# Kernel optimization log

Measured on AMD Instinct MI355X. Metric: run time of the kernel, lower is better.

## Reference

```python
import jax, jax.numpy as jnp
import numpy as np

B, T, N, F = 8, 32, 10000, 16
E = 160000
HG, HT = 64, 128
EPS = 1e-5


def setup_inputs() -> dict:
    key = jax.random.key(0)
    ks = jax.random.split(key, 12)
    s = lambda i, shape, sc=0.05: jax.random.normal(ks[i], shape, dtype=jnp.float32) * sc
    return {
        "x_seq": jax.random.normal(ks[0], (B, T, N, F), dtype=jnp.float32),
        "edge_index": jax.random.randint(ks[1], (2, E), 0, N),
        "W1l": s(2, (HG, F)), "b1": jnp.zeros((HG,), jnp.float32), "W1r": s(3, (HG, F)),
        "g1": jnp.ones((HG,), jnp.float32), "be1": jnp.zeros((HG,), jnp.float32),
        "W2l": s(4, (HG, HG)), "b2": jnp.zeros((HG,), jnp.float32), "W2r": s(5, (HG, HG)),
        "g2": jnp.ones((HG,), jnp.float32), "be2": jnp.zeros((HG,), jnp.float32),
        "W_ih": s(6, (3 * HT, HG)), "W_hh": s(7, (3 * HT, HT)),
        "b_ih": jnp.zeros((3 * HT,), jnp.float32), "b_hh": jnp.zeros((3 * HT,), jnp.float32),
        "Wh": s(8, (1, HT)), "bh": jnp.zeros((1,), jnp.float32),
    }


def _layernorm(h, g, b):
    mu = h.mean(-1, keepdims=True)
    var = ((h - mu) ** 2).mean(-1, keepdims=True)
    return (h - mu) * jax.lax.rsqrt(var + EPS) * g + b


def reference(x_seq, edge_index, W1l, b1, W1r, g1, be1, W2l, b2, W2r, g2, be2,
              W_ih, W_hh, b_ih, b_hh, Wh, bh):
    src, dst = edge_index[0], edge_index[1]
    deg = jax.ops.segment_sum(jnp.ones((E,), x_seq.dtype), dst, num_segments=N)
    inv_deg = (1.0 / jnp.maximum(deg, 1.0))[:, None]  # [N,1]

    def aggregate(x):  # x: [B,N,F] -> mean over incoming neighbors per node
        msgs = x[:, src, :]  # [B,E,F] gather
        agg = jax.vmap(lambda m: jax.ops.segment_sum(m, dst, num_segments=N))(msgs)
        return agg * inv_deg

    def sage(x, Wl, bl, Wr, g, b):
        # PyG SAGEConv(mean): lin_l(agg) + lin_r(x); then LayerNorm + ReLU (dropout=eval)
        h = aggregate(x) @ Wl.T + bl + x @ Wr.T
        return jax.nn.relu(_layernorm(h, g, b))

    def step(_, xt):  # xt: [B,N,F] -> pooled [B,HG]
        h = sage(xt, W1l, b1, W1r, g1, be1)
        h = sage(h, W2l, b2, W2r, g2, be2)
        return None, h.mean(axis=1)

    _, H = jax.lax.scan(step, None, jnp.swapaxes(x_seq, 0, 1))  # [T,B,HG]

    def gru_step(h, x):  # PyTorch GRU gate order: r, z, n
        gi = x @ W_ih.T + b_ih
        gh = h @ W_hh.T + b_hh
        ir, iz, in_ = jnp.split(gi, 3, axis=-1)
        hr, hz, hn = jnp.split(gh, 3, axis=-1)
        r = jax.nn.sigmoid(ir + hr)
        z = jax.nn.sigmoid(iz + hz)
        n = jnp.tanh(in_ + r * hn)
        return (1.0 - z) * n + z * h, None

    h0 = jnp.zeros((x_seq.shape[0], HT), x_seq.dtype)
    ht, _ = jax.lax.scan(gru_step, h0, H)
    return (ht @ Wh.T + bh).squeeze(-1)  # [B]
```

## Files before the change

### kernel.cpp

```cpp
#include <hip/hip_runtime.h>
#include <hip/hip_fp16.h>
#include <math.h>

#define B_ 8
#define T_ 32
#define N_ 10000
#define F_ 16
#define E_ 160000
#define HG_ 64
#define HT_ 128
#define BT_ (B_*T_)
#define PB_ 157
#define EPS_ 1e-5f
#define NR_ (N_+1)

typedef __attribute__((ext_vector_type(8))) _Float16 f16x8_t;
typedef __attribute__((ext_vector_type(4))) float f32x4_t;

__device__ inline unsigned short f2h(float f) {
  return __half_as_ushort(__float2half(f));
}
__device__ inline unsigned pkrtz_u(float a, float b) {
  auto h = __builtin_amdgcn_cvt_pkrtz(a, b);
  unsigned u; __builtin_memcpy(&u, &h, 4); return u;
}
__device__ inline unsigned pack2h(float a, float b) {
  __half2 h = __floats2half2_rn(a, b);
  unsigned u; __builtin_memcpy(&u, &h, 4); return u;
}
__device__ inline __half2 u2h(unsigned u) {
  __half2 h; __builtin_memcpy(&h, &u, 4); return h;
}
__device__ inline unsigned h2u(__half2 h) {
  unsigned u; __builtin_memcpy(&u, &h, 4); return u;
}
__device__ inline void bflyh(__half2& a, int m) {
  unsigned u = (unsigned)__shfl_xor((int)h2u(a), m);
  a += u2h(u);
}

__global__ void k_zero(int* p, int n) {
  int i = blockIdx.x * 256 + threadIdx.x;
  if (i < n) p[i] = 0;
}

__global__ void k_deg(const int* __restrict__ dst, int* __restrict__ deg) {
  int e = blockIdx.x * 256 + threadIdx.x;
  if (e < E_) atomicAdd(&deg[dst[e]], 1);
}

__global__ void k_scan(const int* __restrict__ deg, int* __restrict__ row_ptr,
                       float* __restrict__ inv_deg) {
  __shared__ int part[256];
  int tid = threadIdx.x;
  int base = tid * 40;
  int s = 0;
  for (int i = 0; i < 40; i++) { int idx = base + i; if (idx < N_) s += deg[idx]; }
  part[tid] = s;
  __syncthreads();
  if (tid == 0) {
    int run = 0;
    for (int i = 0; i < 256; i++) { int v = part[i]; part[i] = run; run += v; }
  }
  __syncthreads();
  int run = part[tid];
  for (int i = 0; i < 40; i++) {
    int idx = base + i;
    if (idx < N_) {
      row_ptr[idx] = run;
      int d = deg[idx];
      run += d;
      inv_deg[idx] = 1.0f / fmaxf((float)d, 1.0f);
    } else if (idx == N_) {
      row_ptr[N_] = run;
    }
  }
}

__global__ void k_fill(const int* __restrict__ src, const int* __restrict__ dst,
                       const int* __restrict__ row_ptr, int* __restrict__ cursor,
                       int* __restrict__ col) {
  int e = blockIdx.x * 256 + threadIdx.x;
  if (e < E_) {
    int d = dst[e];
    int p = atomicAdd(&cursor[d], 1);
    col[row_ptr[d] + p] = src[e];
  }
}

__global__ void k_prepw(const float* __restrict__ W2l, const float* __restrict__ W2r,
                        unsigned short* __restrict__ Wbf) {
  int idx = blockIdx.x * 256 + threadIdx.x;
  if (idx >= 4 * 4 * 64 * 8) return;
  int q  = idx & 7;
  int l  = (idx >> 3) & 63;
  int ks = (idx >> 9) & 3;
  int w  = idx >> 11;
  int j = w * 16 + (l & 15);
  int k = ks * 32 + ((l >> 4) * 8) + q;
  float v = (k < 64) ? W2l[j * 64 + k] : W2r[j * 64 + (k - 64)];
  Wbf[idx] = f2h(v);
}

__global__ void k_prepw1(const float* __restrict__ W1l, const float* __restrict__ W1r,
                         unsigned short* __restrict__ Wb1) {
  int idx = blockIdx.x * 256 + threadIdx.x;
  if (idx >= 4 * 64 * 8) return;
  int q = idx & 7;
  int l = (idx >> 3) & 63;
  int w = idx >> 9;
  int j = w * 16 + (l & 15);
  int k = ((l >> 4) * 8) + q;
  float v = (k < 16) ? W1l[j * 16 + k] : W1r[j * 16 + (k - 16)];
  Wb1[idx] = f2h(v);
}

__launch_bounds__(256, 8)
__global__ void k_sage1t(const float* __restrict__ x, const int* __restrict__ row_ptr,
                         const int* __restrict__ col, const float* __restrict__ inv_deg,
                         const unsigned short* __restrict__ Wb1, const float* __restrict__ b1,
                         const float* __restrict__ g1, const float* __restrict__ be1,
                         unsigned short* __restrict__ h1, const float* __restrict__ zrow,
                         int bt0, int CH, int swz) {
  __shared__ __align__(16) unsigned short ZU[64 * 136];
  __shared__ float red[2][4][64];
  unsigned short* Z1b = ZU;
  float* Zf = (float*)ZU;
  int i = blockIdx.x;
  int btl, chunk;
  if (swz) {
    int xcd = i & 7; int j = i >> 3; int per = CH >> 3;
    btl = xcd * per + j / PB_; chunk = j % PB_;
  } else {
    btl = i / PB_; chunk = i % PB_;
  }
  int bt = bt0 + btl;
  size_t xbase = (size_t)bt * (N_ * F_);
  int tid = threadIdx.x;
  int w = __builtin_amdgcn_readfirstlane(tid >> 6);
  int lane = tid & 63;
  int n0 = chunk * 64;
  int node = lane >> 4;
  int eo2 = (lane >> 2) & 3;
  int fq2 = lane & 3;
  const float4* x4b = (const float4*)(x + xbase);
  const float4* z4 = (const float4*)zrow;

  int nloc = n0 + w * 16 + (lane & 15);
  int rpA = 0, dS = 0; float ivS = 0.f;
  if (nloc < N_) { rpA = row_ptr[nloc]; dS = row_ptr[nloc + 1] - rpA; ivS = inv_deg[nloc]; }

  for (int p = 0; p < 4; ++p) {
    int mA = w * 16 + p * 4;
    int nA = n0 + mA;
    int s0My   = __shfl(rpA, p * 4 + node);
    int dMy    = __shfl(dS,  p * 4 + node);
    float ivMy = __shfl(ivS, p * 4 + node);
    int dcMy = dMy > 64 ? 64 : dMy;
    int tmx = max(dcMy, __shfl_xor(dcMy, 16));
    int mx  = max(tmx, __shfl_xor(tmx, 32));
    int rounds = (mx + 3) >> 2;
    int pos = lane & 15;
    int c0r = (pos      < dMy) ? col[s0My + pos]      : 0;
    int c1r = (pos + 16 < dMy) ? col[s0My + pos + 16] : 0;
    int c2r = (pos + 32 < dMy) ? col[s0My + pos + 32] : 0;
    int c3r = (pos + 48 < dMy) ? col[s0My + pos + 48] : 0;
    float4 a = {0.f, 0.f, 0.f, 0.f};
#define S1B(REG, BASE, RR)                                            \
    {                                                                 \
      int idx = eo2 + 4 * (RR);                                       \
      int s = __shfl(REG, (lane & 48) | (idx - (BASE)));              \
      const float4* bp = (idx < dcMy) ? (x4b + (size_t)s * 4) : z4;   \
      float4 v = bp[fq2];                                             \
      a.x += v.x; a.y += v.y; a.z += v.z; a.w += v.w;                 \
    }
    int rounds2 = (rounds + 1) & ~1;
    int r = 0;
    for (; r < rounds2 && r < 4;  r += 2) { S1B(c0r, 0, r)  S1B(c0r, 0, r + 1) }
    for (; r < rounds2 && r < 8;  r += 2) { S1B(c1r, 16, r) S1B(c1r, 16, r + 1) }
    for (; r < rounds2 && r < 12; r += 2) { S1B(c2r, 32, r) S1B(c2r, 32, r + 1) }
    for (; r < rounds2; r += 2)           { S1B(c3r, 48, r) S1B(c3r, 48, r + 1) }
#undef S1B
    if (dMy > 64) {
      for (int e = s0My + 64; e < s0My + dMy; ++e) {
        if (eo2 == 0) {
          float4 v = x4b[(size_t)col[e] * 4 + fq2];
          a.x += v.x; a.y += v.y; a.z += v.z; a.w += v.w;
        }
      }
    }
    a.x += __shfl_xor(a.x, 4);  a.y += __shfl_xor(a.y, 4);
    a.z += __shfl_xor(a.z, 4);  a.w += __shfl_xor(a.w, 4);
    a.x += __shfl_xor(a.x, 8);  a.y += __shfl_xor(a.y, 8);
    a.z += __shfl_xor(a.z, 8);  a.w += __shfl_xor(a.w, 8);
    if (eo2 == 0) {
      uint2 pk;
      pk.x = pkrtz_u(a.x * ivMy, a.y * ivMy);
      pk.y = pkrtz_u(a.z * ivMy, a.w * ivMy);
      *(uint2*)&Z1b[(mA + node) * 40 + fq2 * 4] = pk;
    } else if (eo2 == 1) {
      int nS = nA + node;
      float4 sv = {0.f, 0.f, 0.f, 0.f};
      if (nS < N_) sv = x4b[(size_t)nS * 4 + fq2];
      uint2 pk;
      pk.x = pkrtz_u(sv.x, sv.y);
      pk.y = pkrtz_u(sv.z, sv.w);
      *(uint2*)&Z1b[(mA + node) * 40 + 16 + fq2 * 4] = pk;
    }
  }
  __syncthreads();

  int g = lane >> 4, c = lane & 15;
  float bj = b1[w * 16 + c];
  f32x4_t accf[4];
#pragma unroll
  for (int mt = 0; mt < 4; ++mt) accf[mt] = (f32x4_t){bj, bj, bj, bj};
  f16x8_t bfr = ((const f16x8_t*)Wb1)[w * 64 + lane];
#pragma unroll
  for (int mt = 0; mt < 4; ++mt) {
    const f16x8_t* ap = (const f16x8_t*)&Z1b[(mt * 16 + c) * 40 + g * 8];
    accf[mt] = __builtin_amdgcn_mfma_f32_16x16x32_f16(*ap, bfr, accf[mt], 0, 0, 0);
  }
  __syncthreads();

#pragma unroll
  for (int mt = 0; mt < 4; ++mt) {
#pragma unroll
    for (int q = 0; q < 4; ++q) {
      int nodeq = mt * 16 + g * 4 + q;
      Zf[nodeq * 68 + w * 16 + c] = accf[mt][q];
    }
  }
  __syncthreads();

  int m = lane;
  const float* zr = Zf + m * 68 + w * 16;
  float4 z0 = *(const float4*)(zr + 0);
  float4 z1 = *(const float4*)(zr + 4);
  float4 z2 = *(const float4*)(zr + 8);
  float4 z3 = *(const float4*)(zr + 12);
  float acc[16];
  acc[0] = z0.x; acc[1] = z0.y; acc[2] = z0.z; acc[3] = z0.w;
  acc[4] = z1.x; acc[5] = z1.y; acc[6] = z1.z; acc[7] = z1.w;
  acc[8] = z2.x; acc[9] = z2.y; acc[10] = z2.z; acc[11] = z2.w;
  acc[12] = z3.x; acc[13] = z3.y; acc[14] = z3.z; acc[15] = z3.w;

  float s1 = 0.f, s2 = 0.f;
#pragma unroll
  for (int jj = 0; jj < 16; ++jj) { s1 += acc[jj]; s2 += acc[jj] * acc[jj]; }
  red[0][w][m] = s1;
  red[1][w][m] = s2;
  __syncthreads();
  float mu = (red[0][0][m] + red[0][1][m] + red[0][2][m] + red[0][3][m]) * (1.f / 64.f);
  float ex2 = (red[1][0][m] + red[1][1][m] + red[1][2][m] + red[1][3][m]) * (1.f / 64.f);
  float var = fmaxf(ex2 - mu * mu, 0.f);
  float rs = rsqrtf(var + EPS_);

  int nAbs = n0 + m;
  unsigned short* dst = h1 + ((size_t)btl * NR_ + nAbs) * HG_ + w * 16;
  if (nAbs < N_) {
#pragma unroll
    for (int jj = 0; jj < 16; ++jj)
      acc[jj] = fmaxf((acc[jj] - mu) * rs * g1[w * 16 + jj] + be1[w * 16 + jj], 0.f);
    uint4 pa, pb;
    pa.x = pack2h(acc[0], acc[1]);  pa.y = pack2h(acc[2], acc[3]);
    pa.z = pack2h(acc[4], acc[5]);  pa.w = pack2h(acc[6], acc[7]);
    pb.x = pack2h(acc[8], acc[9]);  pb.y = pack2h(acc[10], acc[11]);
    pb.z = pack2h(acc[12], acc[13]); pb.w = pack2h(acc[14], acc[15]);
    *(uint4*)dst = pa;
    *(uint4*)(dst + 8) = pb;
  } else if (nAbs == N_) {
    uint4 zz = {0, 0, 0, 0};
    *(uint4*)dst = zz;
    *(uint4*)(dst + 8) = zz;
  }
}

__launch_bounds__(256, 8)
__global__ void k_sage2t(const unsigned short* __restrict__ h1, const int* __restrict__ row_ptr,
                         const int* __restrict__ col, const float* __restrict__ inv_deg,
                         const unsigned short* __restrict__ Wbf, const float* __restrict__ b2,
                         const float* __restrict__ g2, const float* __restrict__ be2,
                         float* __restrict__ Hsum, int bt0, int CH, int swz) {
  __shared__ __align__(16) unsigned short Zb[64 * 136];
  __shared__ float red[2][4][64];
  float* Zf = (float*)Zb;
  int i = blockIdx.x;
  int btl, chunk;
  if (swz) {
    int xcd = i & 7; int j = i >> 3; int per = CH >> 3;
    btl = xcd * per + j / PB_; chunk = j % PB_;
  } else {
    btl = i / PB_; chunk = i % PB_;
  }
  int bt = bt0 + btl;
  int b = bt / T_, t = bt % T_;
  const char* h8c = (const char*)(h1 + (size_t)btl * (NR_ * HG_));
  int tid = threadIdx.x;
  int w = __builtin_amdgcn_readfirstlane(tid >> 6);
  int lane = tid & 63;
  int n0 = chunk * 64;
  int nsel = lane >> 5;
  int eo2 = (lane >> 3) & 3;
  int fq3 = lane & 7;
  unsigned foff = (unsigned)fq3 * 16;
  int pos = lane & 31;

  int nloc = n0 + w * 16 + (lane & 15);
  int rpA = 0, dS = 0; float ivS = 0.f;
  if (nloc < N_) { rpA = row_ptr[nloc]; dS = row_ptr[nloc + 1] - rpA; ivS = inv_deg[nloc]; }

  int cp0[8], cp1[8];
#pragma unroll
  for (int p = 0; p < 8; ++p) {
    int s0 = __shfl(rpA, p * 2 + nsel);
    int d  = __shfl(dS,  p * 2 + nsel);
    cp0[p] = (pos      < d) ? col[s0 + pos]      : N_;
    cp1[p] = (pos + 32 < d) ? col[s0 + pos + 32] : N_;
  }

#pragma unroll
  for (int p = 0; p < 8; ++p) {
    int mA = w * 16 + p * 2;
    int s0My   = __shfl(rpA, p * 2 + nsel);
    int dMy    = __shfl(dS,  p * 2 + nsel);
    float ivMy = __shfl(ivS, p * 2 + nsel);
    int dcMy = dMy > 64 ? 64 : dMy;
    int mx = max(dcMy, __shfl_xor(dcMy, 32));
    int rounds = (mx + 3) >> 2;
    __half2 a0 = __float2half2_rn(0.f), a1 = a0, a2 = a0, a3 = a0;
#define S2B(PREG, BASE, RR)                                             \
    {                                                                   \
      int idx = eo2 + 4 * (RR);                                         \
      int s = __shfl(PREG, (lane & 32) | (idx - (BASE)));               \
      uint4 v = *(const uint4*)(h8c + (((unsigned)s << 7) + foff));     \
      a0 += u2h(v.x); a1 += u2h(v.y); a2 += u2h(v.z); a3 += u2h(v.w);   \
    }
    int rounds2 = (rounds + 1) & ~1;
    int r = 0;
    for (; r < rounds2 && r < 8; r += 2) { S2B(cp0[p], 0, r)  S2B(cp0[p], 0, r + 1) }
    for (; r < rounds2; r += 2)          { S2B(cp1[p], 32, r) S2B(cp1[p], 32, r + 1) }
#undef S2B
    if (dMy > 64) {
      for (int e = s0My + 64; e < s0My + dMy; ++e) {
        if (eo2 == 0) {
          uint4 v = *(const uint4*)(h8c + (((unsigned)col[e] << 7) + foff));
          a0 += u2h(v.x); a1 += u2h(v.y); a2 += u2h(v.z); a3 += u2h(v.w);
        }
      }
    }
    bflyh(a0, 8);  bflyh(a1, 8);  bflyh(a2, 8);  bflyh(a3, 8);
    bflyh(a0, 16); bflyh(a1, 16); bflyh(a2, 16); bflyh(a3, 16);
    if (eo2 == 0) {
      __half2 ivh = __float2half2_rn(ivMy);
      uint4 pk;
      pk.x = h2u(a0 * ivh); pk.y = h2u(a1 * ivh);
      pk.z = h2u(a2 * ivh); pk.w = h2u(a3 * ivh);
      *(uint4*)&Zb[(mA + nsel) * 136 + fq3 * 8] = pk;
    } else if (eo2 == 1) {
      int nA = n0 + mA;
      int nS = nA + nsel;
      int nSc = nS < N_ ? nS : N_;
      uint4 sv = *(const uint4*)(h8c + (((unsigned)nSc << 7) + foff));
      *(uint4*)&Zb[(mA + nsel) * 136 + 64 + fq3 * 8] = sv;
    }
  }
  __syncthreads();

  int g = lane >> 4, c = lane & 15;
  const f16x8_t* Wb8 = (const f16x8_t*)Wbf;
  float bj = b2[w * 16 + c];
  f32x4_t accf[4];
#pragma unroll
  for (int mt = 0; mt < 4; ++mt) accf[mt] = (f32x4_t){bj, bj, bj, bj};
#pragma unroll
  for (int ks = 0; ks < 4; ++ks) {
    f16x8_t bfr = Wb8[(w * 4 + ks) * 64 + lane];
#pragma unroll
    for (int mt = 0; mt < 4; ++mt) {
      const f16x8_t* ap = (const f16x8_t*)&Zb[(mt * 16 + c) * 136 + ks * 32 + g * 8];
      accf[mt] = __builtin_amdgcn_mfma_f32_16x16x32_f16(*ap, bfr, accf[mt], 0, 0, 0);
    }
  }
  __syncthreads();

#pragma unroll
  for (int mt = 0; mt < 4; ++mt) {
#pragma unroll
    for (int q = 0; q < 4; ++q) {
      int nodeq = mt * 16 + g * 4 + q;
      Zf[nodeq * 68 + w * 16 + c] = accf[mt][q];
    }
  }
  __syncthreads();

  int m = lane;
  float* zr = Zf + m * 68 + w * 16;
  float4 z0 = *(const float4*)(zr + 0);
  float4 z1 = *(const float4*)(zr + 4);
  float4 z2 = *(const float4*)(zr + 8);
  float4 z3 = *(const float4*)(zr + 12);
  float acc[16];
  acc[0] = z0.x; acc[1] = z0.y; acc[2] = z0.z; acc[3] = z0.w;
  acc[4] = z1.x; acc[5] = z1.y; acc[6] = z1.z; acc[7] = z1.w;
  acc[8] = z2.x; acc[9] = z2.y; acc[10] = z2.z; acc[11] = z2.w;
  acc[12] = z3.x; acc[13] = z3.y; acc[14] = z3.z; acc[15] = z3.w;

  float s1 = 0.f, s2 = 0.f;
#pragma unroll
  for (int jj = 0; jj < 16; ++jj) { s1 += acc[jj]; s2 += acc[jj] * acc[jj]; }
  red[0][w][m] = s1;
  red[1][w][m] = s2;
  __syncthreads();
  float mu = (red[0][0][m] + red[0][1][m] + red[0][2][m] + red[0][3][m]) * (1.f / 64.f);
  float ex2 = (red[1][0][m] + red[1][1][m] + red[1][2][m] + red[1][3][m]) * (1.f / 64.f);
  float var = fmaxf(ex2 - mu * mu, 0.f);
  float rs = rsqrtf(var + EPS_);

  bool okm = (n0 + m) < N_;
#pragma unroll
  for (int jj = 0; jj < 16; ++jj) {
    float hv = fmaxf((acc[jj] - mu) * rs * g2[w * 16 + jj] + be2[w * 16 + jj], 0.f);
    acc[jj] = okm ? hv : 0.f;
  }
  float4 o0 = {acc[0], acc[1], acc[2], acc[3]};
  float4 o1 = {acc[4], acc[5], acc[6], acc[7]};
  float4 o2 = {acc[8], acc[9], acc[10], acc[11]};
  float4 o3 = {acc[12], acc[13], acc[14], acc[15]};
  *(float4*)(zr + 0) = o0;  *(float4*)(zr + 4) = o1;
  *(float4*)(zr + 8) = o2;  *(float4*)(zr + 12) = o3;
  __syncthreads();

  float cs = 0.f;
#pragma unroll
  for (int ii = 0; ii < 16; ++ii) cs += Zf[(w * 16 + ii) * 68 + lane];
  red[0][w][lane] = cs;
  __syncthreads();
  if (w == 0) {
    float tot = red[0][0][lane] + red[0][1][lane] + red[0][2][lane] + red[0][3][lane];
    atomicAdd(&Hsum[(t * B_ + b) * HG_ + lane], tot);
  }
}

__global__ void k_gi(const float* __restrict__ Hsum, const float* __restrict__ W_ih,
                     const float* __restrict__ b_ih, float* __restrict__ GI) {
  __shared__ float xv[64];
  int tb = blockIdx.x;
  int tid = threadIdx.x;
  if (tid < 64) xv[tid] = Hsum[tb * 64 + tid] * (1.0f / (float)N_);
  __syncthreads();
  float g = b_ih[tid];
  const float4* W4 = (const float4*)(W_ih + tid * 64);
  const float4* x4 = (const float4*)xv;
#pragma unroll
  for (int q = 0; q < 16; q++) {
    float4 w = W4[q], xq = x4[q];
    g = fmaf(xq.x, w.x, g); g = fmaf(xq.y, w.y, g);
    g = fmaf(xq.z, w.z, g); g = fmaf(xq.w, w.w, g);
  }
  GI[tb * 384 + tid] = g;
}

__global__ void k_gru(const float* __restrict__ GI, const float* __restrict__ W_hh,
                      const float* __restrict__ b_hh, const float* __restrict__ Wh,
                      const float* __restrict__ bh, float* __restrict__ out) {
  __shared__ float hL[128];
  __shared__ float ghL[384];
  __shared__ float red[128];
  int b = blockIdx.x, tid = threadIdx.x;
  if (tid < 128) hL[tid] = 0.f;
  float bhh = b_hh[tid];
  const float4* W4 = (const float4*)(W_hh + tid * 128);
  for (int t = 0; t < T_; ++t) {
    __syncthreads();
    float g = bhh;
    const float4* h4 = (const float4*)hL;
#pragma unroll
    for (int q = 0; q < 32; q++) {
      float4 w = W4[q], hv = h4[q];
      g = fmaf(hv.x, w.x, g); g = fmaf(hv.y, w.y, g);
      g = fmaf(hv.z, w.z, g); g = fmaf(hv.w, w.w, g);
    }
    ghL[tid] = g;
    __syncthreads();
    float hnew = 0.f;
    if (tid < 128) {
      const float* gi = GI + (t * B_ + b) * 384;
      float rr = 1.f / (1.f + expf(-(gi[tid] + ghL[tid])));
      float zz = 1.f / (1.f + expf(-(gi[128 + tid] + ghL[128 + tid])));
      float nn = tanhf(gi[256 + tid] + rr * ghL[256 + tid]);
      hnew = (1.f - zz) * nn + zz * hL[tid];
    }
    __syncthreads();
    if (tid < 128) hL[tid] = hnew;
  }
  __syncthreads();
  if (tid < 128) red[tid] = hL[tid] * Wh[tid];
  __syncthreads();
  if (tid == 0) {
    float s = bh[0];
    for (int k = 0; k < 128; k++) s += red[k];
    out[b] = s;
  }
}

extern "C" void kernel_launch(void* const* d_in, const int* in_sizes, int n_in,
                              void* d_out, int out_size, void* d_ws, size_t ws_size,
                              hipStream_t stream) {
  const float* x    = (const float*)d_in[0];
  const int*   ei   = (const int*)d_in[1];
  const float* W1l  = (const float*)d_in[2];
  const float* b1   = (const float*)d_in[3];
  const float* W1r  = (const float*)d_in[4];
  const float* g1   = (const float*)d_in[5];
  const float* be1  = (const float*)d_in[6];
  const float* W2l  = (const float*)d_in[7];
  const float* b2   = (const float*)d_in[8];
  const float* W2r  = (const float*)d_in[9];
  const float* g2   = (const float*)d_in[10];
  const float* be2  = (const float*)d_in[11];
  const float* W_ih = (const float*)d_in[12];
  const float* W_hh = (const float*)d_in[13];
  const float* b_ih = (const float*)d_in[14];
  const float* b_hh = (const float*)d_in[15];
  const float* Wh   = (const float*)d_in[16];
  const float* bh   = (const float*)d_in[17];
  float* out = (float*)d_out;

  char* ws = (char*)d_ws;
  size_t off = 0;
  auto alloc = [&](size_t bytes) { void* p = ws + off; off += (bytes + 255) & ~(size_t)255; return p; };
  int*   deg     = (int*)alloc((size_t)N_ * 4);
  int*   row_ptr = (int*)alloc((size_t)(N_ + 1) * 4);
  int*   cursor  = (int*)alloc((size_t)N_ * 4);
  int*   col     = (int*)alloc((size_t)E_ * 4);
  float* ivd     = (float*)alloc((size_t)N_ * 4);
  float* Hsum    = (float*)alloc((size_t)BT_ * HG_ * 4);
  float* GI      = (float*)alloc((size_t)BT_ * 384 * 4);
  unsigned short* Wbf = (unsigned short*)alloc((size_t)4 * 4 * 64 * 8 * 2);
  unsigned short* Wb1 = (unsigned short*)alloc((size_t)4 * 64 * 8 * 2);
  float* zrowp   = (float*)alloc(256);
  size_t fixed = off;
  unsigned short* h1 = (unsigned short*)(ws + off);

  size_t cap = (ws_size > fixed) ? (ws_size - fixed) : 0;
  int CH = (int)(cap / ((size_t)NR_ * HG_ * 2));
  if (CH > 64) CH = 64;
  if (CH >= 8) CH &= ~7;
  if (CH < 1) CH = 1;

  int zn = (int)(fixed / 4);
  k_zero<<<(zn + 255) / 256, 256, 0, stream>>>((int*)ws, zn);

  const int* srcp = ei;
  const int* dstp = ei + E_;
  k_deg<<<(E_ + 255) / 256, 256, 0, stream>>>(dstp, deg);
  k_scan<<<1, 256, 0, stream>>>(deg, row_ptr, ivd);
  k_fill<<<(E_ + 255) / 256, 256, 0, stream>>>(srcp, dstp, row_ptr, cursor, col);
  k_prepw<<<32, 256, 0, stream>>>(W2l, W2r, Wbf);
  k_prepw1<<<8, 256, 0, stream>>>(W1l, W1r, Wb1);

  for (int bt0 = 0; bt0 < BT_; bt0 += CH) {
    int c = BT_ - bt0 < CH ? BT_ - bt0 : CH;
    int swz = (c % 8 == 0) ? 1 : 0;
    k_sage1t<<<c * PB_, 256, 0, stream>>>(x, row_ptr, col, ivd, Wb1, b1, g1, be1,
                                          h1, zrowp, bt0, c, swz);
    k_sage2t<<<c * PB_, 256, 0, stream>>>(h1, row_ptr, col, ivd, Wbf, b2, g2, be2,
                                          Hsum, bt0, c, swz);
  }
  k_gi<<<BT_, 384, 0, stream>>>(Hsum, W_ih, b_ih, GI);
  k_gru<<<B_, 384, 0, stream>>>(GI, W_hh, b_hh, Wh, bh, out);
}
```

Baseline: 1.164 ms.

## Process one node per wavefront in neighbor gathers, drop padded zero row

Both SAGE gather kernels now handle one destination node at a time per wavefront, spreading its edges across all lanes, instead of packing several nodes per wavefront with padded rounds up to the max degree. The dummy zero row (N+1 layout) and zrow pointer are removed in favor of predicated loads. The block-to-XCD swizzle now interleaves bt slices across XCDs instead of giving each XCD a contiguous range. This aims to cut wasted loads from degree imbalance and padding, but serializes 16 nodes per wave and adds extra butterfly reductions per node, which lowers memory-level parallelism at the average degree of 16.

```diff
diff --git a/kernel.cpp b/kernel.cpp
--- a/kernel.cpp
+++ b/kernel.cpp
@@ -12,7 +12,6 @@
 #define BT_ (B_*T_)
 #define PB_ 157
 #define EPS_ 1e-5f
-#define NR_ (N_+1)
 
 typedef __attribute__((ext_vector_type(8))) _Float16 f16x8_t;
 typedef __attribute__((ext_vector_type(4))) float f32x4_t;
@@ -116,97 +115,68 @@
 }
 
 __launch_bounds__(256, 8)
-__global__ void k_sage1t(const float* __restrict__ x, const int* __restrict__ row_ptr,
-                         const int* __restrict__ col, const float* __restrict__ inv_deg,
-                         const unsigned short* __restrict__ Wb1, const float* __restrict__ b1,
-                         const float* __restrict__ g1, const float* __restrict__ be1,
-                         unsigned short* __restrict__ h1, const float* __restrict__ zrow,
-                         int bt0, int CH, int swz) {
+__global__ void k_s1(const float* __restrict__ x, const int* __restrict__ row_ptr,
+                     const int* __restrict__ col, const float* __restrict__ inv_deg,
+                     const unsigned short* __restrict__ Wb1, const float* __restrict__ b1,
+                     const float* __restrict__ g1, const float* __restrict__ be1,
+                     unsigned short* __restrict__ h1, int bt0, int swz) {
   __shared__ __align__(16) unsigned short ZU[64 * 136];
   __shared__ float red[2][4][64];
   unsigned short* Z1b = ZU;
   float* Zf = (float*)ZU;
   int i = blockIdx.x;
   int btl, chunk;
-  if (swz) {
-    int xcd = i & 7; int j = i >> 3; int per = CH >> 3;
-    btl = xcd * per + j / PB_; chunk = j % PB_;
-  } else {
-    btl = i / PB_; chunk = i % PB_;
-  }
+  if (swz) { int xcd = i & 7; int jj = i >> 3; btl = (jj / PB_) * 8 + xcd; chunk = jj % PB_; }
+  else     { btl = i / PB_; chunk = i % PB_; }
   int bt = bt0 + btl;
-  size_t xbase = (size_t)bt * (N_ * F_);
+  const float4* xb = (const float4*)(x + (size_t)bt * (N_ * F_));
   int tid = threadIdx.x;
   int w = __builtin_amdgcn_readfirstlane(tid >> 6);
   int lane = tid & 63;
   int n0 = chunk * 64;
-  int node = lane >> 4;
-  int eo2 = (lane >> 2) & 3;
-  int fq2 = lane & 3;
-  const float4* x4b = (const float4*)(x + xbase);
-  const float4* z4 = (const float4*)zrow;
+  int fq2 = lane & 3, e4 = lane >> 2;
 
   int nloc = n0 + w * 16 + (lane & 15);
-  int rpA = 0, dS = 0; float ivS = 0.f;
-  if (nloc < N_) { rpA = row_ptr[nloc]; dS = row_ptr[nloc + 1] - rpA; ivS = inv_deg[nloc]; }
-
-  for (int p = 0; p < 4; ++p) {
-    int mA = w * 16 + p * 4;
-    int nA = n0 + mA;
-    int s0My   = __shfl(rpA, p * 4 + node);
-    int dMy    = __shfl(dS,  p * 4 + node);
-    float ivMy = __shfl(ivS, p * 4 + node);
-    int dcMy = dMy > 64 ? 64 : dMy;
-    int tmx = max(dcMy, __shfl_xor(dcMy, 16));
-    int mx  = max(tmx, __shfl_xor(tmx, 32));
-    int rounds = (mx + 3) >> 2;
-    int pos = lane & 15;
-    int c0r = (pos      < dMy) ? col[s0My + pos]      : 0;
-    int c1r = (pos + 16 < dMy) ? col[s0My + pos + 16] : 0;
-    int c2r = (pos + 32 < dMy) ? col[s0My + pos + 32] : 0;
-    int c3r = (pos + 48 < dMy) ? col[s0My + pos + 48] : 0;
-    float4 a = {0.f, 0.f, 0.f, 0.f};
-#define S1B(REG, BASE, RR)                                            \
-    {                                                                 \
-      int idx = eo2 + 4 * (RR);                                       \
-      int s = __shfl(REG, (lane & 48) | (idx - (BASE)));              \
-      const float4* bp = (idx < dcMy) ? (x4b + (size_t)s * 4) : z4;   \
-      float4 v = bp[fq2];                                             \
-      a.x += v.x; a.y += v.y; a.z += v.z; a.w += v.w;                 \
-    }
-    int rounds2 = (rounds + 1) & ~1;
-    int r = 0;
-    for (; r < rounds2 && r < 4;  r += 2) { S1B(c0r, 0, r)  S1B(c0r, 0, r + 1) }
-    for (; r < rounds2 && r < 8;  r += 2) { S1B(c1r, 16, r) S1B(c1r, 16, r + 1) }
-    for (; r < rounds2 && r < 12; r += 2) { S1B(c2r, 32, r) S1B(c2r, 32, r + 1) }
-    for (; r < rounds2; r += 2)           { S1B(c3r, 48, r) S1B(c3r, 48, r + 1) }
-#undef S1B
-    if (dMy > 64) {
-      for (int e = s0My + 64; e < s0My + dMy; ++e) {
-        if (eo2 == 0) {
-          float4 v = x4b[(size_t)col[e] * 4 + fq2];
-          a.x += v.x; a.y += v.y; a.z += v.z; a.w += v.w;
+  int rp = 0, dS = 0; float ivS = 0.f;
+  if (nloc < N_) { rp = row_ptr[nloc]; dS = row_ptr[nloc + 1] - rp; ivS = inv_deg[nloc]; }
+
+  for (int nn = 0; nn < 16; ++nn) {
+    int s0 = __shfl(rp, nn), dd = __shfl(dS, nn);
+    float iv = __shfl(ivS, nn);
+    float4 acc = {0.f, 0.f, 0.f, 0.f};
+    for (int base = 0; base < dd; base += 64) {
+      int cnt = dd - base; if (cnt > 64) cnt = 64;
+      int cl = (lane < cnt) ? col[s0 + base + lane] : 0;
+      for (int e = 0; e < cnt; e += 16) {
+        int idx = e + e4;
+        int s = __shfl(cl, idx);
+        if (idx < cnt) {
+          float4 v = xb[(size_t)s * 4 + fq2];
+          acc.x += v.x; acc.y += v.y; acc.z += v.z; acc.w += v.w;
         }
       }
     }
-    a.x += __shfl_xor(a.x, 4);  a.y += __shfl_xor(a.y, 4);
-    a.z += __shfl_xor(a.z, 4);  a.w += __shfl_xor(a.w, 4);
-    a.x += __shfl_xor(a.x, 8);  a.y += __shfl_xor(a.y, 8);
-    a.z += __shfl_xor(a.z, 8);  a.w += __shfl_xor(a.w, 8);
-    if (eo2 == 0) {
+#pragma unroll
+    for (int mk = 4; mk < 64; mk <<= 1) {
+      acc.x += __shfl_xor(acc.x, mk); acc.y += __shfl_xor(acc.y, mk);
+      acc.z += __shfl_xor(acc.z, mk); acc.w += __shfl_xor(acc.w, mk);
+    }
+    if (e4 == 0) {
       uint2 pk;
-      pk.x = pkrtz_u(a.x * ivMy, a.y * ivMy);
-      pk.y = pkrtz_u(a.z * ivMy, a.w * ivMy);
-      *(uint2*)&Z1b[(mA + node) * 40 + fq2 * 4] = pk;
-    } else if (eo2 == 1) {
-      int nS = nA + node;
-      float4 sv = {0.f, 0.f, 0.f, 0.f};
-      if (nS < N_) sv = x4b[(size_t)nS * 4 + fq2];
-      uint2 pk;
-      pk.x = pkrtz_u(sv.x, sv.y);
-      pk.y = pkrtz_u(sv.z, sv.w);
-      *(uint2*)&Z1b[(mA + node) * 40 + 16 + fq2 * 4] = pk;
-    }
+      pk.x = pkrtz_u(acc.x * iv, acc.y * iv);
+      pk.y = pkrtz_u(acc.z * iv, acc.w * iv);
+      *(uint2*)&Z1b[(w * 16 + nn) * 40 + fq2 * 4] = pk;
+    }
+  }
+  {
+    int m = w * 16 + (lane >> 2);
+    int ng = n0 + m;
+    float4 sv = {0.f, 0.f, 0.f, 0.f};
+    if (ng < N_) sv = xb[(size_t)ng * 4 + fq2];
+    uint2 pk;
+    pk.x = pkrtz_u(sv.x, sv.y);
+    pk.y = pkrtz_u(sv.z, sv.w);
+    *(uint2*)&Z1b[m * 40 + 16 + fq2 * 4] = pk;
   }
   __syncthreads();
 
@@ -257,7 +227,6 @@
   float rs = rsqrtf(var + EPS_);
 
   int nAbs = n0 + m;
-  unsigned short* dst = h1 + ((size_t)btl * NR_ + nAbs) * HG_ + w * 16;
   if (nAbs < N_) {
 #pragma unroll
     for (int jj = 0; jj < 16; ++jj)
@@ -267,103 +236,73 @@
     pa.z = pack2h(acc[4], acc[5]);  pa.w = pack2h(acc[6], acc[7]);
     pb.x = pack2h(acc[8], acc[9]);  pb.y = pack2h(acc[10], acc[11]);
     pb.z = pack2h(acc[12], acc[13]); pb.w = pack2h(acc[14], acc[15]);
+    unsigned short* dst = h1 + ((size_t)btl * N_ + nAbs) * HG_ + w * 16;
     *(uint4*)dst = pa;
     *(uint4*)(dst + 8) = pb;
-  } else if (nAbs == N_) {
-    uint4 zz = {0, 0, 0, 0};
-    *(uint4*)dst = zz;
-    *(uint4*)(dst + 8) = zz;
   }
 }
 
 __launch_bounds__(256, 8)
-__global__ void k_sage2t(const unsigned short* __restrict__ h1, const int* __restrict__ row_ptr,
-                         const int* __restrict__ col, const float* __restrict__ inv_deg,
-                         const unsigned short* __restrict__ Wbf, const float* __restrict__ b2,
-                         const float* __restrict__ g2, const float* __restrict__ be2,
-                         float* __restrict__ Hsum, int bt0, int CH, int swz) {
+__global__ void k_s2(const unsigned short* __restrict__ h1, const int* __restrict__ row_ptr,
+                     const int* __restrict__ col, const float* __restrict__ inv_deg,
+                     const unsigned short* __restrict__ Wbf, const float* __restrict__ b2,
+                     const float* __restrict__ g2, const float* __restrict__ be2,
+                     float* __restrict__ Hsum, int bt0, int swz) {
   __shared__ __align__(16) unsigned short Zb[64 * 136];
   __shared__ float red[2][4][64];
   float* Zf = (float*)Zb;
   int i = blockIdx.x;
   int btl, chunk;
-  if (swz) {
-    int xcd = i & 7; int j = i >> 3; int per = CH >> 3;
-    btl = xcd * per + j / PB_; chunk = j % PB_;
-  } else {
-    btl = i / PB_; chunk = i % PB_;
-  }
+  if (swz) { int xcd = i & 7; int jj = i >> 3; btl = (jj / PB_) * 8 + xcd; chunk = jj % PB_; }
+  else     { btl = i / PB_; chunk = i % PB_; }
   int bt = bt0 + btl;
   int b = bt / T_, t = bt % T_;
-  const char* h8c = (const char*)(h1 + (size_t)btl * (NR_ * HG_));
+  const char* hb = (const char*)(h1 + (size_t)btl * ((size_t)N_ * HG_));
   int tid = threadIdx.x;
   int w = __builtin_amdgcn_readfirstlane(tid >> 6);
   int lane = tid & 63;
   int n0 = chunk * 64;
-  int nsel = lane >> 5;
-  int eo2 = (lane >> 3) & 3;
-  int fq3 = lane & 7;
+  int fq3 = lane & 7, e3 = lane >> 3;
   unsigned foff = (unsigned)fq3 * 16;
-  int pos = lane & 31;
 
   int nloc = n0 + w * 16 + (lane & 15);
-  int rpA = 0, dS = 0; float ivS = 0.f;
-  if (nloc < N_) { rpA = row_ptr[nloc]; dS = row_ptr[nloc + 1] - rpA; ivS = inv_deg[nloc]; }
-
-  int cp0[8], cp1[8];
-#pragma unroll
-  for (int p = 0; p < 8; ++p) {
-    int s0 = __shfl(rpA, p * 2 + nsel);
-    int d  = __shfl(dS,  p * 2 + nsel);
-    cp0[p] = (pos      < d) ? col[s0 + pos]      : N_;
-    cp1[p] = (pos + 32 < d) ? col[s0 + pos + 32] : N_;
-  }
-
-#pragma unroll
-  for (int p = 0; p < 8; ++p) {
-    int mA = w * 16 + p * 2;
-    int s0My   = __shfl(rpA, p * 2 + nsel);
-    int dMy    = __shfl(dS,  p * 2 + nsel);
-    float ivMy = __shfl(ivS, p * 2 + nsel);
-    int dcMy = dMy > 64 ? 64 : dMy;
-    int mx = max(dcMy, __shfl_xor(dcMy, 32));
-    int rounds = (mx + 3) >> 2;
+  int rp = 0, dS = 0; float ivS = 0.f;
+  if (nloc < N_) { rp = row_ptr[nloc]; dS = row_ptr[nloc + 1] - rp; ivS = inv_deg[nloc]; }
+
+  for (int nn = 0; nn < 16; ++nn) {
+    int s0 = __shfl(rp, nn), dd = __shfl(dS, nn);
+    float iv = __shfl(ivS, nn);
     __half2 a0 = __float2half2_rn(0.f), a1 = a0, a2 = a0, a3 = a0;
-#define S2B(PREG, BASE, RR)                                             \
-    {                                                                   \
-      int idx = eo2 + 4 * (RR);                                         \
-      int s = __shfl(PREG, (lane & 32) | (idx - (BASE)));               \
-      uint4 v = *(const uint4*)(h8c + (((unsigned)s << 7) + foff));     \
-      a0 += u2h(v.x); a1 += u2h(v.y); a2 += u2h(v.z); a3 += u2h(v.w);   \
-    }
-    int rounds2 = (rounds + 1) & ~1;
-    int r = 0;
-    for (; r < rounds2 && r < 8; r += 2) { S2B(cp0[p], 0, r)  S2B(cp0[p], 0, r + 1) }
-    for (; r < rounds2; r += 2)          { S2B(cp1[p], 32, r) S2B(cp1[p], 32, r + 1) }
-#undef S2B
-    if (dMy > 64) {
-      for (int e = s0My + 64; e < s0My + dMy; ++e) {
-        if (eo2 == 0) {
-          uint4 v = *(const uint4*)(h8c + (((unsigned)col[e] << 7) + foff));
+    for (int base = 0; base < dd; base += 64) {
+      int cnt = dd - base; if (cnt > 64) cnt = 64;
+      int cl = (lane < cnt) ? col[s0 + base + lane] : 0;
+      for (int e = 0; e < cnt; e += 8) {
+        int idx = e + e3;
+        int s = __shfl(cl, idx);
+        if (idx < cnt) {
+          uint4 v = *(const uint4*)(hb + (((size_t)s) << 7) + foff);
           a0 += u2h(v.x); a1 += u2h(v.y); a2 += u2h(v.z); a3 += u2h(v.w);
         }
       }
     }
     bflyh(a0, 8);  bflyh(a1, 8);  bflyh(a2, 8);  bflyh(a3, 8);
     bflyh(a0, 16); bflyh(a1, 16); bflyh(a2, 16); bflyh(a3, 16);
-    if (eo2 == 0) {
-      __half2 ivh = __float2half2_rn(ivMy);
+    bflyh(a0, 32); bflyh(a1, 32); bflyh(a2, 32); bflyh(a3, 32);
+    if (e3 == 0) {
+      __half2 ivh = __float2half2_rn(iv);
       uint4 pk;
       pk.x = h2u(a0 * ivh); pk.y = h2u(a1 * ivh);
       pk.z = h2u(a2 * ivh); pk.w = h2u(a3 * ivh);
-      *(uint4*)&Zb[(mA + nsel) * 136 + fq3 * 8] = pk;
-    } else if (eo2 == 1) {
-      int nA = n0 + mA;
-      int nS = nA + nsel;
-      int nSc = nS < N_ ? nS : N_;
-      uint4 sv = *(const uint4*)(h8c + (((unsigned)nSc << 7) + foff));
-      *(uint4*)&Zb[(mA + nsel) * 136 + 64 + fq3 * 8] = sv;
-    }
+      *(uint4*)&Zb[(w * 16 + nn) * 136 + fq3 * 8] = pk;
+    }
+  }
+#pragma unroll
+  for (int p = 0; p < 2; ++p) {
+    int m = w * 16 + p * 8 + e3;
+    int ng = n0 + m;
+    uint4 sv = {0, 0, 0, 0};
+    if (ng < N_) sv = *(const uint4*)(hb + (((size_t)ng) << 7) + foff);
+    *(uint4*)&Zb[m * 136 + 64 + fq3 * 8] = sv;
   }
   __syncthreads();
 
@@ -539,12 +478,12 @@
   float* GI      = (float*)alloc((size_t)BT_ * 384 * 4);
   unsigned short* Wbf = (unsigned short*)alloc((size_t)4 * 4 * 64 * 8 * 2);
   unsigned short* Wb1 = (unsigned short*)alloc((size_t)4 * 64 * 8 * 2);
-  float* zrowp   = (float*)alloc(256);
   size_t fixed = off;
   unsigned short* h1 = (unsigned short*)(ws + off);
 
+  size_t slab = (size_t)N_ * HG_ * 2;
   size_t cap = (ws_size > fixed) ? (ws_size - fixed) : 0;
-  int CH = (int)(cap / ((size_t)NR_ * HG_ * 2));
+  int CH = (int)(cap / slab);
   if (CH > 64) CH = 64;
   if (CH >= 8) CH &= ~7;
   if (CH < 1) CH = 1;
@@ -563,10 +502,10 @@
   for (int bt0 = 0; bt0 < BT_; bt0 += CH) {
     int c = BT_ - bt0 < CH ? BT_ - bt0 : CH;
     int swz = (c % 8 == 0) ? 1 : 0;
-    k_sage1t<<<c * PB_, 256, 0, stream>>>(x, row_ptr, col, ivd, Wb1, b1, g1, be1,
-                                          h1, zrowp, bt0, c, swz);
-    k_sage2t<<<c * PB_, 256, 0, stream>>>(h1, row_ptr, col, ivd, Wbf, b2, g2, be2,
-                                          Hsum, bt0, c, swz);
+    k_s1<<<c * PB_, 256, 0, stream>>>(x, row_ptr, col, ivd, Wb1, b1, g1, be1,
+                                      h1, bt0, swz);
+    k_s2<<<c * PB_, 256, 0, stream>>>(h1, row_ptr, col, ivd, Wbf, b2, g2, be2,
+                                      Hsum, bt0, swz);
   }
   k_gi<<<BT_, 384, 0, stream>>>(Hsum, W_ih, b_ih, GI);
   k_gru<<<B_, 384, 0, stream>>>(GI, W_hh, b_hh, Wh, bh, out);
```

Result: slower. 1.678 ms (+44.1%).

## Precompute padded per-lane neighbor offset tables for SAGE gather loops

Applied to the files above, without the earlier changes.

Adds preprocessing kernels that compute per-group round counts, prefix-scan them, and build padded tables of pre-scaled neighbor byte offsets laid out in the exact lane order the aggregation loops consume. The two SAGE kernels then read offsets straight from these tables instead of loading row_ptr/col, doing shuffles, and handling the >64-degree tail separately. This removes index-shuffle overhead and degree-dependent branching from the hot gather loops. The cost is extra setup kernels, more workspace (which shrinks the chunk capacity CH slightly), and extra table reads per round.

```diff
diff --git a/kernel.cpp b/kernel.cpp
--- a/kernel.cpp
+++ b/kernel.cpp
@@ -13,6 +13,8 @@
 #define PB_ 157
 #define EPS_ 1e-5f
 #define NR_ (N_+1)
+#define NG1_ (PB_*4*4)
+#define NG2_ (PB_*4*8)
 
 typedef __attribute__((ext_vector_type(8))) _Float16 f16x8_t;
 typedef __attribute__((ext_vector_type(4))) float f32x4_t;
@@ -85,6 +87,96 @@
     int d = dst[e];
     int p = atomicAdd(&cursor[d], 1);
     col[row_ptr[d] + p] = src[e];
+  }
+}
+
+__global__ void k_trounds1(const int* __restrict__ row_ptr, int* __restrict__ cnt1) {
+  int g = blockIdx.x * 256 + threadIdx.x;
+  if (g >= NG1_) return;
+  int c = g >> 4, w = (g >> 2) & 3, p = g & 3;
+  int nb = c * 64 + w * 16 + p * 4;
+  int mx = 0;
+#pragma unroll
+  for (int k = 0; k < 4; ++k) {
+    int n = nb + k;
+    int d = (n < N_) ? (row_ptr[n + 1] - row_ptr[n]) : 0;
+    mx = max(mx, d);
+  }
+  cnt1[g] = ((mx + 3) >> 2) * 16;
+}
+
+__global__ void k_trounds2(const int* __restrict__ row_ptr, int* __restrict__ cnt2) {
+  int g = blockIdx.x * 256 + threadIdx.x;
+  if (g >= NG2_) return;
+  int c = g >> 5, w = (g >> 3) & 3, p = g & 7;
+  int nb = c * 64 + w * 16 + p * 2;
+  int mx = 0;
+#pragma unroll
+  for (int k = 0; k < 2; ++k) {
+    int n = nb + k;
+    int d = (n < N_) ? (row_ptr[n + 1] - row_ptr[n]) : 0;
+    mx = max(mx, d);
+  }
+  cnt2[g] = ((mx + 3) >> 2) * 8;
+}
+
+__global__ void k_pscan(const int* __restrict__ cnt, int* __restrict__ off, int n) {
+  __shared__ int part[256];
+  int tid = threadIdx.x;
+  int per = (n + 255) / 256;
+  int base = tid * per;
+  int s = 0;
+  for (int i = 0; i < per; i++) { int idx = base + i; if (idx < n) s += cnt[idx]; }
+  part[tid] = s;
+  __syncthreads();
+  if (tid == 0) {
+    int run = 0;
+    for (int i = 0; i < 256; i++) { int v = part[i]; part[i] = run; run += v; }
+    off[n] = run;
+  }
+  __syncthreads();
+  int run = part[tid];
+  for (int i = 0; i < per; i++) {
+    int idx = base + i;
+    if (idx < n) { off[idx] = run; run += cnt[idx]; }
+  }
+}
+
+__global__ void k_tfill1(const int* __restrict__ row_ptr, const int* __restrict__ col,
+                         const int* __restrict__ toff1, int* __restrict__ T1) {
+  int idx = blockIdx.x * 256 + threadIdx.x;
+  if (idx >= NG1_ * 16) return;
+  int g = idx >> 4, slot = idx & 15;
+  int node2 = slot >> 2, eo2 = slot & 3;
+  int c = g >> 4, w = (g >> 2) & 3, p = g & 3;
+  int n = c * 64 + w * 16 + p * 4 + node2;
+  int s0 = 0, d = 0;
+  if (n < N_) { s0 = row_ptr[n]; d = row_ptr[n + 1] - s0; }
+  int o = toff1[g];
+  int nr = (toff1[g + 1] - o) >> 4;
+  int* tb = T1 + o + slot;
+  for (int r = 0; r < nr; ++r) {
+    int e = eo2 + 4 * r;
+    tb[r * 16] = (e < d) ? col[s0 + e] * 64 : -64;
+  }
+}
+
+__global__ void k_tfill2(const int* __restrict__ row_ptr, const int* __restrict__ col,
+                         const int* __restrict__ toff2, int* __restrict__ T2) {
+  int idx = blockIdx.x * 256 + threadIdx.x;
+  if (idx >= NG2_ * 8) return;
+  int g = idx >> 3, slot = idx & 7;
+  int nsel = slot >> 2, eo2 = slot & 3;
+  int c = g >> 5, w = (g >> 3) & 3, p = g & 7;
+  int n = c * 64 + w * 16 + p * 2 + nsel;
+  int s0 = 0, d = 0;
+  if (n < N_) { s0 = row_ptr[n]; d = row_ptr[n + 1] - s0; }
+  int o = toff2[g];
+  int nr = (toff2[g + 1] - o) >> 3;
+  int* tb = T2 + o + slot;
+  for (int r = 0; r < nr; ++r) {
+    int e = eo2 + 4 * r;
+    tb[r * 8] = (e < d) ? col[s0 + e] * 128 : N_ * 128;
   }
 }
 
@@ -116,8 +208,8 @@
 }
 
 __launch_bounds__(256, 8)
-__global__ void k_sage1t(const float* __restrict__ x, const int* __restrict__ row_ptr,
-                         const int* __restrict__ col, const float* __restrict__ inv_deg,
+__global__ void k_sage1t(const float* __restrict__ x, const float* __restrict__ inv_deg,
+                         const int* __restrict__ toff1, const int* __restrict__ T1,
                          const unsigned short* __restrict__ Wb1, const float* __restrict__ b1,
                          const float* __restrict__ g1, const float* __restrict__ be1,
                          unsigned short* __restrict__ h1, const float* __restrict__ zrow,
@@ -135,7 +227,6 @@
     btl = i / PB_; chunk = i % PB_;
   }
   int bt = bt0 + btl;
-  size_t xbase = (size_t)bt * (N_ * F_);
   int tid = threadIdx.x;
   int w = __builtin_amdgcn_readfirstlane(tid >> 6);
   int lane = tid & 63;
@@ -143,51 +234,38 @@
   int node = lane >> 4;
   int eo2 = (lane >> 2) & 3;
   int fq2 = lane & 3;
-  const float4* x4b = (const float4*)(x + xbase);
-  const float4* z4 = (const float4*)zrow;
+  const float4* xb = (const float4*)(x + (size_t)bt * (N_ * F_));
+  const char* xbF = (const char*)xb + fq2 * 16;
+  const char* zF = (const char*)zrow + fq2 * 16;
 
   int nloc = n0 + w * 16 + (lane & 15);
-  int rpA = 0, dS = 0; float ivS = 0.f;
-  if (nloc < N_) { rpA = row_ptr[nloc]; dS = row_ptr[nloc + 1] - rpA; ivS = inv_deg[nloc]; }
+  float ivS = (nloc < N_) ? inv_deg[nloc] : 0.f;
+  int gidb = (chunk * 4 + w) * 4;
+  int toS = (lane <= 4) ? toff1[gidb + lane] : 0;
 
   for (int p = 0; p < 4; ++p) {
     int mA = w * 16 + p * 4;
     int nA = n0 + mA;
-    int s0My   = __shfl(rpA, p * 4 + node);
-    int dMy    = __shfl(dS,  p * 4 + node);
     float ivMy = __shfl(ivS, p * 4 + node);
-    int dcMy = dMy > 64 ? 64 : dMy;
-    int tmx = max(dcMy, __shfl_xor(dcMy, 16));
-    int mx  = max(tmx, __shfl_xor(tmx, 32));
-    int rounds = (mx + 3) >> 2;
-    int pos = lane & 15;
-    int c0r = (pos      < dMy) ? col[s0My + pos]      : 0;
-    int c1r = (pos + 16 < dMy) ? col[s0My + pos + 16] : 0;
-    int c2r = (pos + 32 < dMy) ? col[s0My + pos + 32] : 0;
-    int c3r = (pos + 48 < dMy) ? col[s0My + pos + 48] : 0;
+    int o0 = __shfl(toS, p), o1 = __shfl(toS, p + 1);
+    int nr = (o1 - o0) >> 4;
+    const int* tp = T1 + o0 + (lane >> 2);
     float4 a = {0.f, 0.f, 0.f, 0.f};
-#define S1B(REG, BASE, RR)                                            \
-    {                                                                 \
-      int idx = eo2 + 4 * (RR);                                       \
-      int s = __shfl(REG, (lane & 48) | (idx - (BASE)));              \
-      const float4* bp = (idx < dcMy) ? (x4b + (size_t)s * 4) : z4;   \
-      float4 v = bp[fq2];                                             \
-      a.x += v.x; a.y += v.y; a.z += v.z; a.w += v.w;                 \
-    }
-    int rounds2 = (rounds + 1) & ~1;
     int r = 0;
-    for (; r < rounds2 && r < 4;  r += 2) { S1B(c0r, 0, r)  S1B(c0r, 0, r + 1) }
-    for (; r < rounds2 && r < 8;  r += 2) { S1B(c1r, 16, r) S1B(c1r, 16, r + 1) }
-    for (; r < rounds2 && r < 12; r += 2) { S1B(c2r, 32, r) S1B(c2r, 32, r + 1) }
-    for (; r < rounds2; r += 2)           { S1B(c3r, 48, r) S1B(c3r, 48, r + 1) }
-#undef S1B
-    if (dMy > 64) {
-      for (int e = s0My + 64; e < s0My + dMy; ++e) {
-        if (eo2 == 0) {
-          float4 v = x4b[(size_t)col[e] * 4 + fq2];
-          a.x += v.x; a.y += v.y; a.z += v.z; a.w += v.w;
-        }
-      }
+    for (; r + 1 < nr; r += 2) {
+      int sa = tp[r * 16], sb = tp[r * 16 + 16];
+      const char* pa = (sa >= 0) ? (xbF + sa) : zF;
+      const char* pb = (sb >= 0) ? (xbF + sb) : zF;
+      float4 va = *(const float4*)pa;
+      float4 vb = *(const float4*)pb;
+      a.x += va.x; a.y += va.y; a.z += va.z; a.w += va.w;
+      a.x += vb.x; a.y += vb.y; a.z += vb.z; a.w += vb.w;
+    }
+    if (r < nr) {
+      int sa = tp[r * 16];
+      const char* pa = (sa >= 0) ? (xbF + sa) : zF;
+      float4 va = *(const float4*)pa;
+      a.x += va.x; a.y += va.y; a.z += va.z; a.w += va.w;
     }
     a.x += __shfl_xor(a.x, 4);  a.y += __shfl_xor(a.y, 4);
     a.z += __shfl_xor(a.z, 4);  a.w += __shfl_xor(a.w, 4);
@@ -201,7 +279,7 @@
     } else if (eo2 == 1) {
       int nS = nA + node;
       float4 sv = {0.f, 0.f, 0.f, 0.f};
-      if (nS < N_) sv = x4b[(size_t)nS * 4 + fq2];
+      if (nS < N_) sv = xb[(size_t)nS * 4 + fq2];
       uint2 pk;
       pk.x = pkrtz_u(sv.x, sv.y);
       pk.y = pkrtz_u(sv.z, sv.w);
@@ -277,8 +355,8 @@
 }
 
 __launch_bounds__(256, 8)
-__global__ void k_sage2t(const unsigned short* __restrict__ h1, const int* __restrict__ row_ptr,
-                         const int* __restrict__ col, const float* __restrict__ inv_deg,
+__global__ void k_sage2t(const unsigned short* __restrict__ h1, const float* __restrict__ inv_deg,
+                         const int* __restrict__ toff2, const int* __restrict__ T2,
                          const unsigned short* __restrict__ Wbf, const float* __restrict__ b2,
                          const float* __restrict__ g2, const float* __restrict__ be2,
                          float* __restrict__ Hsum, int bt0, int CH, int swz) {
@@ -295,62 +373,43 @@
   }
   int bt = bt0 + btl;
   int b = bt / T_, t = bt % T_;
-  const char* h8c = (const char*)(h1 + (size_t)btl * (NR_ * HG_));
+  const char* hb = (const char*)(h1 + (size_t)btl * ((size_t)NR_ * HG_));
   int tid = threadIdx.x;
   int w = __builtin_amdgcn_readfirstlane(tid >> 6);
   int lane = tid & 63;
   int n0 = chunk * 64;
   int nsel = lane >> 5;
-  int eo2 = (lane >> 3) & 3;
   int fq3 = lane & 7;
-  unsigned foff = (unsigned)fq3 * 16;
-  int pos = lane & 31;
+  const char* hbF = hb + fq3 * 16;
 
   int nloc = n0 + w * 16 + (lane & 15);
-  int rpA = 0, dS = 0; float ivS = 0.f;
-  if (nloc < N_) { rpA = row_ptr[nloc]; dS = row_ptr[nloc + 1] - rpA; ivS = inv_deg[nloc]; }
-
-  int cp0[8], cp1[8];
-#pragma unroll
-  for (int p = 0; p < 8; ++p) {
-    int s0 = __shfl(rpA, p * 2 + nsel);
-    int d  = __shfl(dS,  p * 2 + nsel);
-    cp0[p] = (pos      < d) ? col[s0 + pos]      : N_;
-    cp1[p] = (pos + 32 < d) ? col[s0 + pos + 32] : N_;
-  }
-
-#pragma unroll
+  float ivS = (nloc < N_) ? inv_deg[nloc] : 0.f;
+  int gidb = (chunk * 4 + w) * 8;
+  int toS = (lane <= 8) ? toff2[gidb + lane] : 0;
+
   for (int p = 0; p < 8; ++p) {
     int mA = w * 16 + p * 2;
-    int s0My   = __shfl(rpA, p * 2 + nsel);
-    int dMy    = __shfl(dS,  p * 2 + nsel);
     float ivMy = __shfl(ivS, p * 2 + nsel);
-    int dcMy = dMy > 64 ? 64 : dMy;
-    int mx = max(dcMy, __shfl_xor(dcMy, 32));
-    int rounds = (mx + 3) >> 2;
+    int o0 = __shfl(toS, p), o1 = __shfl(toS, p + 1);
+    int nr = (o1 - o0) >> 3;
+    const int* tp = T2 + o0 + (lane >> 3);
     __half2 a0 = __float2half2_rn(0.f), a1 = a0, a2 = a0, a3 = a0;
-#define S2B(PREG, BASE, RR)                                             \
-    {                                                                   \
-      int idx = eo2 + 4 * (RR);                                         \
-      int s = __shfl(PREG, (lane & 32) | (idx - (BASE)));               \
-      uint4 v = *(const uint4*)(h8c + (((unsigned)s << 7) + foff));     \
-      a0 += u2h(v.x); a1 += u2h(v.y); a2 += u2h(v.z); a3 += u2h(v.w);   \
-    }
-    int rounds2 = (rounds + 1) & ~1;
     int r = 0;
-    for (; r < rounds2 && r < 8; r += 2) { S2B(cp0[p], 0, r)  S2B(cp0[p], 0, r + 1) }
-    for (; r < rounds2; r += 2)          { S2B(cp1[p], 32, r) S2B(cp1[p], 32, r + 1) }
-#undef S2B
-    if (dMy > 64) {
-      for (int e = s0My + 64; e < s0My + dMy; ++e) {
-        if (eo2 == 0) {
-          uint4 v = *(const uint4*)(h8c + (((unsigned)col[e] << 7) + foff));
-          a0 += u2h(v.x); a1 += u2h(v.y); a2 += u2h(v.z); a3 += u2h(v.w);
-        }
-      }
+    for (; r + 1 < nr; r += 2) {
+      int sa = tp[r * 8], sb = tp[r * 8 + 8];
+      uint4 va = *(const uint4*)(hbF + sa);
+      uint4 vb = *(const uint4*)(hbF + sb);
+      a0 += u2h(va.x); a1 += u2h(va.y); a2 += u2h(va.z); a3 += u2h(va.w);
+      a0 += u2h(vb.x); a1 += u2h(vb.y); a2 += u2h(vb.z); a3 += u2h(vb.w);
+    }
+    if (r < nr) {
+      int sa = tp[r * 8];
+      uint4 va = *(const uint4*)(hbF + sa);
+      a0 += u2h(va.x); a1 += u2h(va.y); a2 += u2h(va.z); a3 += u2h(va.w);
     }
     bflyh(a0, 8);  bflyh(a1, 8);  bflyh(a2, 8);  bflyh(a3, 8);
     bflyh(a0, 16); bflyh(a1, 16); bflyh(a2, 16); bflyh(a3, 16);
+    int eo2 = (lane >> 3) & 3;
     if (eo2 == 0) {
       __half2 ivh = __float2half2_rn(ivMy);
       uint4 pk;
@@ -358,10 +417,9 @@
       pk.z = h2u(a2 * ivh); pk.w = h2u(a3 * ivh);
       *(uint4*)&Zb[(mA + nsel) * 136 + fq3 * 8] = pk;
     } else if (eo2 == 1) {
-      int nA = n0 + mA;
-      int nS = nA + nsel;
+      int nS = n0 + mA + nsel;
       int nSc = nS < N_ ? nS : N_;
-      uint4 sv = *(const uint4*)(h8c + (((unsigned)nSc << 7) + foff));
+      uint4 sv = *(const uint4*)(hbF + ((size_t)nSc << 7));
       *(uint4*)&Zb[(mA + nsel) * 136 + 64 + fq3 * 8] = sv;
     }
   }
@@ -540,11 +598,18 @@
   unsigned short* Wbf = (unsigned short*)alloc((size_t)4 * 4 * 64 * 8 * 2);
   unsigned short* Wb1 = (unsigned short*)alloc((size_t)4 * 64 * 8 * 2);
   float* zrowp   = (float*)alloc(256);
+  int*   cnt1    = (int*)alloc((size_t)NG1_ * 4);
+  int*   cnt2    = (int*)alloc((size_t)NG2_ * 4);
+  int*   toff1   = (int*)alloc((size_t)(NG1_ + 1) * 4);
+  int*   toff2   = (int*)alloc((size_t)(NG2_ + 1) * 4);
+  int*   T1      = (int*)alloc(((size_t)E_ / 4 + NG1_) * 16 * 4);
+  int*   T2      = (int*)alloc(((size_t)E_ / 4 + NG2_) * 8 * 4);
   size_t fixed = off;
   unsigned short* h1 = (unsigned short*)(ws + off);
 
+  size_t slab = (size_t)NR_ * HG_ * 2;
   size_t cap = (ws_size > fixed) ? (ws_size - fixed) : 0;
-  int CH = (int)(cap / ((size_t)NR_ * HG_ * 2));
+  int CH = (int)(cap / slab);
   if (CH > 64) CH = 64;
   if (CH >= 8) CH &= ~7;
   if (CH < 1) CH = 1;
@@ -557,15 +622,21 @@
   k_deg<<<(E_ + 255) / 256, 256, 0, stream>>>(dstp, deg);
   k_scan<<<1, 256, 0, stream>>>(deg, row_ptr, ivd);
   k_fill<<<(E_ + 255) / 256, 256, 0, stream>>>(srcp, dstp, row_ptr, cursor, col);
+  k_trounds1<<<(NG1_ + 255) / 256, 256, 0, stream>>>(row_ptr, cnt1);
+  k_trounds2<<<(NG2_ + 255) / 256, 256, 0, stream>>>(row_ptr, cnt2);
+  k_pscan<<<1, 256, 0, stream>>>(cnt1, toff1, NG1_);
+  k_pscan<<<1, 256, 0, stream>>>(cnt2, toff2, NG2_);
+  k_tfill1<<<(NG1_ * 16 + 255) / 256, 256, 0, stream>>>(row_ptr, col, toff1, T1);
+  k_tfill2<<<(NG2_ * 8 + 255) / 256, 256, 0, stream>>>(row_ptr, col, toff2, T2);
   k_prepw<<<32, 256, 0, stream>>>(W2l, W2r, Wbf);
   k_prepw1<<<8, 256, 0, stream>>>(W1l, W1r, Wb1);
 
   for (int bt0 = 0; bt0 < BT_; bt0 += CH) {
     int c = BT_ - bt0 < CH ? BT_ - bt0 : CH;
     int swz = (c % 8 == 0) ? 1 : 0;
-    k_sage1t<<<c * PB_, 256, 0, stream>>>(x, row_ptr, col, ivd, Wb1, b1, g1, be1,
+    k_sage1t<<<c * PB_, 256, 0, stream>>>(x, ivd, toff1, T1, Wb1, b1, g1, be1,
                                           h1, zrowp, bt0, c, swz);
-    k_sage2t<<<c * PB_, 256, 0, stream>>>(h1, row_ptr, col, ivd, Wbf, b2, g2, be2,
+    k_sage2t<<<c * PB_, 256, 0, stream>>>(h1, ivd, toff2, T2, Wbf, b2, g2, be2,
                                           Hsum, bt0, c, swz);
   }
   k_gi<<<BT_, 384, 0, stream>>>(Hsum, W_ih, b_ih, GI);
```

Measured after the change: 1.249 ms. +7.3%, slower.
